# Optimization experiments

Hardware: AMD Instinct MI355X
Metric: run time of the kernel (lower is better)

## Reference

```python
import jax, jax.numpy as jnp
import numpy as np

NUM_CODES = 512
DIM = 64
B, M = 32, 64


def setup_inputs() -> dict:
    key = jax.random.key(0)
    k1, k2 = jax.random.split(key)
    inputs = jax.random.normal(k1, (B, M, M, DIM), dtype=jnp.float32)
    # keras 'uniform' initializer is U(-0.05, 0.05)
    embeddings = jax.random.uniform(k2, (NUM_CODES, DIM), dtype=jnp.float32,
                                    minval=-0.05, maxval=0.05)
    return {"inputs": inputs, "embeddings": embeddings}


def reference(inputs, embeddings):
    l2_inputs = jnp.sum(inputs * inputs, axis=-1, keepdims=True)      # [B,M,M,1]
    l2_embeddings = jnp.sum(embeddings * embeddings, axis=-1)          # [K]
    dot = jnp.einsum('bhwd,kd->bhwk', inputs, embeddings)              # [B,M,M,K]
    distance = l2_inputs + l2_embeddings - 2.0 * dot                   # [B,M,M,K]
    codes = jnp.argmin(distance, axis=-1).astype(jnp.int32)            # [B,M,M]
    code_vecs = embeddings[codes]                                      # [B,M,M,D]
    return codes, code_vecs
```

## Files before the change

kernel.cpp:

```cpp
#include <hip/hip_runtime.h>

#define NUM_CODES 512
#define DIM 64
#define NPIX (32 * 64 * 64)
#define CT (NUM_CODES / 16)
#define BLK 256
#define PPB 64

typedef __attribute__((ext_vector_type(8))) short bf16x8;
typedef __attribute__((ext_vector_type(4))) float f32x4;

__device__ __forceinline__ unsigned short f2bf(float f) {
    unsigned u = __float_as_uint(f);
    return (unsigned short)((u + 0x7fffu + ((u >> 16) & 1u)) >> 16);
}
__device__ __forceinline__ float bf2f(unsigned short h) {
    return __uint_as_float(((unsigned)h) << 16);
}

__global__ __launch_bounds__(256) void prep_kernel(
    const float* __restrict__ emb, unsigned short* __restrict__ AH,
    unsigned short* __restrict__ ALO, float* __restrict__ l2e,
    float* __restrict__ l2eh) {
    const int t = blockIdx.x * 256 + threadIdx.x;
    const int e0 = t * 4;
    const int c = e0 >> 6, d0 = e0 & 63;
    const float4 v = *(const float4*)(emb + c * DIM + d0);
    float f[4] = {v.x, v.y, v.z, v.w};
    unsigned short h[4], l[4];
#pragma unroll
    for (int i = 0; i < 4; ++i) {
        h[i] = f2bf(f[i]);
        l[i] = f2bf(f[i] - bf2f(h[i]));
    }
    const int ct = c >> 4, mr = c & 15, s = d0 >> 5, q = (d0 & 31) >> 3,
              j0 = d0 & 7;
    const int base = ((ct * 2 + s) * 64 + (q * 16 + mr)) * 8 + j0;
    *(ushort4*)(AH + base) = make_ushort4(h[0], h[1], h[2], h[3]);
    *(ushort4*)(ALO + base) = make_ushort4(l[0], l[1], l[2], l[3]);

    if (t < NUM_CODES) {
        const float* e = emb + t * DIM;
        float r[8];
#pragma unroll
        for (int j = 0; j < 8; ++j) {
            float w = e[j];
            r[j] = w * w;
        }
#pragma unroll
        for (int i = 8; i < DIM; i += 8)
#pragma unroll
            for (int j = 0; j < 8; ++j) {
                float w = e[i + j];
                r[j] += w * w;
            }
        float sv =
            ((r[0] + r[1]) + (r[2] + r[3])) + ((r[4] + r[5]) + (r[6] + r[7]));
        l2e[t] = sv;
        l2eh[t] = 0.5f * sv;
    }
}

__global__ __launch_bounds__(BLK) void vq_main(
    const float* __restrict__ x_in, const unsigned short* __restrict__ AH,
    const unsigned short* __restrict__ ALO, const float* __restrict__ l2e,
    const float* __restrict__ l2eh, const float* __restrict__ emb,
    float* __restrict__ codes_out, float* __restrict__ vecs_out) {
    __shared__ float s_l2eh[NUM_CODES];
    __shared__ float s_l2ex[NUM_CODES];
    __shared__ int s_top[PPB][2];
    __shared__ int s_code[PPB];

    const int tid = threadIdx.x, lane = tid & 63, wave = tid >> 6;
    s_l2eh[tid] = l2eh[tid];
    s_l2eh[tid + 256] = l2eh[tid + 256];
    s_l2ex[tid] = l2e[tid];
    s_l2ex[tid + 256] = l2e[tid + 256];
    __syncthreads();

    const int pg = blockIdx.x * PPB + wave * 16;
    const int p = lane & 15, q = lane >> 4;

    const float* xb = x_in + (size_t)(pg + p) * DIM + q * 8;
    float4 u0 = *(const float4*)(xb);
    float4 u1 = *(const float4*)(xb + 4);
    float4 u2 = *(const float4*)(xb + 32);
    float4 u3 = *(const float4*)(xb + 36);
    float f0[8] = {u0.x, u0.y, u0.z, u0.w, u1.x, u1.y, u1.z, u1.w};
    float f1[8] = {u2.x, u2.y, u2.z, u2.w, u3.x, u3.y, u3.z, u3.w};
    bf16x8 b0h, b0l, b1h, b1l;
#pragma unroll
    for (int j = 0; j < 8; ++j) {
        unsigned short hh = f2bf(f0[j]);
        b0h[j] = (short)hh;
        b0l[j] = (short)f2bf(f0[j] - bf2f(hh));
        unsigned short h2 = f2bf(f1[j]);
        b1h[j] = (short)h2;
        b1l[j] = (short)f2bf(f1[j] - bf2f(h2));
    }

    const int rowbase = q * 4;
    float d1 = 3.4e38f, d2 = 3.4e38f;
    int k1 = 0, k2 = 0;

    const unsigned short* pAH = AH + lane * 8;
    const unsigned short* pAL = ALO + lane * 8;
    for (int ct = 0; ct < CT; ++ct) {
        bf16x8 a0h = *(const bf16x8*)(pAH + ct * 1024);
        bf16x8 a0l = *(const bf16x8*)(pAL + ct * 1024);
        bf16x8 a1h = *(const bf16x8*)(pAH + ct * 1024 + 512);
        bf16x8 a1l = *(const bf16x8*)(pAL + ct * 1024 + 512);
        f32x4 acc = {0.f, 0.f, 0.f, 0.f};
        acc = __builtin_amdgcn_mfma_f32_16x16x32_bf16(a0h, b0h, acc, 0, 0, 0);
        acc = __builtin_amdgcn_mfma_f32_16x16x32_bf16(a1h, b1h, acc, 0, 0, 0);
        acc = __builtin_amdgcn_mfma_f32_16x16x32_bf16(a0l, b0h, acc, 0, 0, 0);
        acc = __builtin_amdgcn_mfma_f32_16x16x32_bf16(a1l, b1h, acc, 0, 0, 0);
        acc = __builtin_amdgcn_mfma_f32_16x16x32_bf16(a0h, b0l, acc, 0, 0, 0);
        acc = __builtin_amdgcn_mfma_f32_16x16x32_bf16(a1h, b1l, acc, 0, 0, 0);

        const int kb = ct * 16 + rowbase;
#pragma unroll
        for (int r = 0; r < 4; ++r) {
            const float d = s_l2eh[kb + r] - acc[r];
            const int kk = kb + r;
            const bool c = d < d1, c2 = d < d2;
            const float nd2 = c2 ? d : d2;
            const int nk2 = c2 ? kk : k2;
            d2 = c ? d1 : nd2;
            k2 = c ? k1 : nk2;
            k1 = c ? kk : k1;
            d1 = c ? d : d1;
        }
    }

#pragma unroll
    for (int off = 16; off <= 32; off <<= 1) {
        const float od1 = __shfl_xor(d1, off);
        const int ok1 = __shfl_xor(k1, off);
        const float od2 = __shfl_xor(d2, off);
        const int ok2 = __shfl_xor(k2, off);
        const bool c = od1 < d1;
        const float w1 = c ? od1 : d1;
        const int wk1 = c ? ok1 : k1;
        const float l1 = c ? d1 : od1;
        const int lk1 = c ? k1 : ok1;
        const bool cm = od2 < d2;
        const float m2 = cm ? od2 : d2;
        const int mk2 = cm ? ok2 : k2;
        const bool c3 = m2 < l1;
        d2 = c3 ? m2 : l1;
        k2 = c3 ? mk2 : lk1;
        d1 = w1;
        k1 = wk1;
    }
    if (lane < 16) {
        s_top[wave * 16 + lane][0] = k1;
        s_top[wave * 16 + lane][1] = k2;
    }
    __syncthreads();

    if (tid < PPB) {
        const int pix = blockIdx.x * PPB + tid;
        int ka = s_top[tid][0], kb2 = s_top[tid][1];
        if (kb2 < ka) {
            const int tt = ka;
            ka = kb2;
            kb2 = tt;
        }
        const float* xr = x_in + (size_t)pix * DIM;
        float x[DIM];
#pragma unroll
        for (int jj = 0; jj < 16; ++jj) {
            const float4 v = *(const float4*)(xr + jj * 4);
            x[4 * jj + 0] = v.x;
            x[4 * jj + 1] = v.y;
            x[4 * jj + 2] = v.z;
            x[4 * jj + 3] = v.w;
        }
        float r[8];
#pragma unroll
        for (int j = 0; j < 8; ++j) r[j] = x[j] * x[j];
#pragma unroll
        for (int i = 8; i < DIM; i += 8)
#pragma unroll
            for (int j = 0; j < 8; ++j) r[j] += x[i + j] * x[i + j];
        const float l2x =
            ((r[0] + r[1]) + (r[2] + r[3])) + ((r[4] + r[5]) + (r[6] + r[7]));

        const float* ea = emb + (size_t)ka * DIM;
        float acca = 0.f;
#pragma unroll
        for (int d = 0; d < DIM; ++d) acca = __builtin_fmaf(x[d], ea[d], acca);
        const float da = (l2x + s_l2ex[ka]) - 2.0f * acca;

        const float* eb = emb + (size_t)kb2 * DIM;
        float accb = 0.f;
#pragma unroll
        for (int d = 0; d < DIM; ++d) accb = __builtin_fmaf(x[d], eb[d], accb);
        const float db = (l2x + s_l2ex[kb2]) - 2.0f * accb;

        const int sel = (db < da) ? kb2 : ka;
        s_code[tid] = sel;
        codes_out[pix] = (float)sel;
    }
    __syncthreads();

    const float4* emb4 = (const float4*)emb;
    float4* vout4 = (float4*)(vecs_out + (size_t)blockIdx.x * PPB * DIM);
#pragma unroll
    for (int it = 0; it < (PPB * DIM / 4) / BLK; ++it) {
        const int fidx = tid + it * BLK;
        const int pp = fidx >> 4, dd = fidx & 15;
        vout4[fidx] = emb4[(size_t)s_code[pp] * (DIM / 4) + dd];
    }
}

extern "C" void kernel_launch(void* const* d_in, const int* in_sizes, int n_in,
                              void* d_out, int out_size, void* d_ws,
                              size_t ws_size, hipStream_t stream) {
    const float* x_in = (const float*)d_in[0];
    const float* emb = (const float*)d_in[1];

    unsigned short* AH = (unsigned short*)d_ws;
    unsigned short* ALO = AH + NUM_CODES * DIM;
    float* l2e = (float*)(ALO + NUM_CODES * DIM);
    float* l2eh = l2e + NUM_CODES;

    float* codes_out = (float*)d_out;
    float* vecs_out = (float*)d_out + NPIX;

    hipLaunchKernelGGL(prep_kernel, dim3(32), dim3(256), 0, stream, emb, AH,
                       ALO, l2e, l2eh);
    hipLaunchKernelGGL(vq_main, dim3(NPIX / PPB), dim3(BLK), 0, stream, x_in,
                       AH, ALO, l2e, l2eh, emb, codes_out, vecs_out);
}
```

Baseline: 131.7 us.

## Process four pixel groups per wave to reuse codebook fragments across MFMAs

Each wave now handles four 16-pixel groups instead of one, so every codebook A-fragment load and LDS norm read is shared by four groups of MFMAs. The block covers 256 pixels, and all 256 threads take part in the exact fp32 rescoring of the top-2 candidates instead of only 64. This cuts global/L2 traffic for the codebook and idle threads in the refine stage. In exchange, register pressure rises from holding four sets of B fragments and top-2 state, the grid shrinks fourfold, and launch_bounds asks for 2 blocks per SIMD group.

New measurement: 127.9 us. -2.9%, faster.

```diff
diff --git a/kernel.cpp b/kernel.cpp
--- a/kernel.cpp
+++ b/kernel.cpp
@@ -5,7 +5,8 @@
 #define NPIX (32 * 64 * 64)
 #define CT (NUM_CODES / 16)
 #define BLK 256
-#define PPB 64
+#define NGRP 4
+#define PPB 256
 
 typedef __attribute__((ext_vector_type(8))) short bf16x8;
 typedef __attribute__((ext_vector_type(4))) float f32x4;
@@ -61,7 +62,7 @@
     }
 }
 
-__global__ __launch_bounds__(BLK) void vq_main(
+__global__ __launch_bounds__(BLK, 2) void vq_main(
     const float* __restrict__ x_in, const unsigned short* __restrict__ AH,
     const unsigned short* __restrict__ ALO, const float* __restrict__ l2e,
     const float* __restrict__ l2eh, const float* __restrict__ emb,
@@ -78,88 +79,110 @@
     s_l2ex[tid + 256] = l2e[tid + 256];
     __syncthreads();
 
-    const int pg = blockIdx.x * PPB + wave * 16;
     const int p = lane & 15, q = lane >> 4;
-
-    const float* xb = x_in + (size_t)(pg + p) * DIM + q * 8;
-    float4 u0 = *(const float4*)(xb);
-    float4 u1 = *(const float4*)(xb + 4);
-    float4 u2 = *(const float4*)(xb + 32);
-    float4 u3 = *(const float4*)(xb + 36);
-    float f0[8] = {u0.x, u0.y, u0.z, u0.w, u1.x, u1.y, u1.z, u1.w};
-    float f1[8] = {u2.x, u2.y, u2.z, u2.w, u3.x, u3.y, u3.z, u3.w};
-    bf16x8 b0h, b0l, b1h, b1l;
-#pragma unroll
-    for (int j = 0; j < 8; ++j) {
-        unsigned short hh = f2bf(f0[j]);
-        b0h[j] = (short)hh;
-        b0l[j] = (short)f2bf(f0[j] - bf2f(hh));
-        unsigned short h2 = f2bf(f1[j]);
-        b1h[j] = (short)h2;
-        b1l[j] = (short)f2bf(f1[j] - bf2f(h2));
+    const int pw = blockIdx.x * PPB + wave * (16 * NGRP);
+
+    bf16x8 bh0[NGRP], bl0[NGRP], bh1[NGRP], bl1[NGRP];
+#pragma unroll
+    for (int g = 0; g < NGRP; ++g) {
+        const float* xb = x_in + (size_t)(pw + g * 16 + p) * DIM + q * 8;
+        float4 u0 = *(const float4*)(xb);
+        float4 u1 = *(const float4*)(xb + 4);
+        float4 u2 = *(const float4*)(xb + 32);
+        float4 u3 = *(const float4*)(xb + 36);
+        float f0[8] = {u0.x, u0.y, u0.z, u0.w, u1.x, u1.y, u1.z, u1.w};
+        float f1[8] = {u2.x, u2.y, u2.z, u2.w, u3.x, u3.y, u3.z, u3.w};
+#pragma unroll
+        for (int j = 0; j < 8; ++j) {
+            unsigned short hh = f2bf(f0[j]);
+            bh0[g][j] = (short)hh;
+            bl0[g][j] = (short)f2bf(f0[j] - bf2f(hh));
+            unsigned short h2 = f2bf(f1[j]);
+            bh1[g][j] = (short)h2;
+            bl1[g][j] = (short)f2bf(f1[j] - bf2f(h2));
+        }
     }
 
     const int rowbase = q * 4;
-    float d1 = 3.4e38f, d2 = 3.4e38f;
-    int k1 = 0, k2 = 0;
+    float d1[NGRP], d2[NGRP];
+    int k1[NGRP], k2[NGRP];
+#pragma unroll
+    for (int g = 0; g < NGRP; ++g) {
+        d1[g] = 3.4e38f;
+        d2[g] = 3.4e38f;
+        k1[g] = 0;
+        k2[g] = 0;
+    }
 
     const unsigned short* pAH = AH + lane * 8;
     const unsigned short* pAL = ALO + lane * 8;
     for (int ct = 0; ct < CT; ++ct) {
-        bf16x8 a0h = *(const bf16x8*)(pAH + ct * 1024);
-        bf16x8 a0l = *(const bf16x8*)(pAL + ct * 1024);
-        bf16x8 a1h = *(const bf16x8*)(pAH + ct * 1024 + 512);
-        bf16x8 a1l = *(const bf16x8*)(pAL + ct * 1024 + 512);
-        f32x4 acc = {0.f, 0.f, 0.f, 0.f};
-        acc = __builtin_amdgcn_mfma_f32_16x16x32_bf16(a0h, b0h, acc, 0, 0, 0);
-        acc = __builtin_amdgcn_mfma_f32_16x16x32_bf16(a1h, b1h, acc, 0, 0, 0);
-        acc = __builtin_amdgcn_mfma_f32_16x16x32_bf16(a0l, b0h, acc, 0, 0, 0);
-        acc = __builtin_amdgcn_mfma_f32_16x16x32_bf16(a1l, b1h, acc, 0, 0, 0);
-        acc = __builtin_amdgcn_mfma_f32_16x16x32_bf16(a0h, b0l, acc, 0, 0, 0);
-        acc = __builtin_amdgcn_mfma_f32_16x16x32_bf16(a1h, b1l, acc, 0, 0, 0);
-
+        const bf16x8 a0h = *(const bf16x8*)(pAH + ct * 1024);
+        const bf16x8 a0l = *(const bf16x8*)(pAL + ct * 1024);
+        const bf16x8 a1h = *(const bf16x8*)(pAH + ct * 1024 + 512);
+        const bf16x8 a1l = *(const bf16x8*)(pAL + ct * 1024 + 512);
         const int kb = ct * 16 + rowbase;
-#pragma unroll
-        for (int r = 0; r < 4; ++r) {
-            const float d = s_l2eh[kb + r] - acc[r];
-            const int kk = kb + r;
-            const bool c = d < d1, c2 = d < d2;
-            const float nd2 = c2 ? d : d2;
-            const int nk2 = c2 ? kk : k2;
-            d2 = c ? d1 : nd2;
-            k2 = c ? k1 : nk2;
-            k1 = c ? kk : k1;
-            d1 = c ? d : d1;
-        }
-    }
-
-#pragma unroll
-    for (int off = 16; off <= 32; off <<= 1) {
-        const float od1 = __shfl_xor(d1, off);
-        const int ok1 = __shfl_xor(k1, off);
-        const float od2 = __shfl_xor(d2, off);
-        const int ok2 = __shfl_xor(k2, off);
-        const bool c = od1 < d1;
-        const float w1 = c ? od1 : d1;
-        const int wk1 = c ? ok1 : k1;
-        const float l1 = c ? d1 : od1;
-        const int lk1 = c ? k1 : ok1;
-        const bool cm = od2 < d2;
-        const float m2 = cm ? od2 : d2;
-        const int mk2 = cm ? ok2 : k2;
-        const bool c3 = m2 < l1;
-        d2 = c3 ? m2 : l1;
-        k2 = c3 ? mk2 : lk1;
-        d1 = w1;
-        k1 = wk1;
-    }
-    if (lane < 16) {
-        s_top[wave * 16 + lane][0] = k1;
-        s_top[wave * 16 + lane][1] = k2;
+        float l2v[4];
+#pragma unroll
+        for (int r = 0; r < 4; ++r) l2v[r] = s_l2eh[kb + r];
+
+#pragma unroll
+        for (int g = 0; g < NGRP; ++g) {
+            f32x4 acc = {0.f, 0.f, 0.f, 0.f};
+            acc = __builtin_amdgcn_mfma_f32_16x16x32_bf16(a0h, bh0[g], acc, 0, 0, 0);
+            acc = __builtin_amdgcn_mfma_f32_16x16x32_bf16(a1h, bh1[g], acc, 0, 0, 0);
+            acc = __builtin_amdgcn_mfma_f32_16x16x32_bf16(a0l, bh0[g], acc, 0, 0, 0);
+            acc = __builtin_amdgcn_mfma_f32_16x16x32_bf16(a1l, bh1[g], acc, 0, 0, 0);
+            acc = __builtin_amdgcn_mfma_f32_16x16x32_bf16(a0h, bl0[g], acc, 0, 0, 0);
+            acc = __builtin_amdgcn_mfma_f32_16x16x32_bf16(a1h, bl1[g], acc, 0, 0, 0);
+
+#pragma unroll
+            for (int r = 0; r < 4; ++r) {
+                const float d = l2v[r] - acc[r];
+                const int kk = kb + r;
+                const bool c = d < d1[g], c2 = d < d2[g];
+                const float nd2 = c2 ? d : d2[g];
+                const int nk2 = c2 ? kk : k2[g];
+                d2[g] = c ? d1[g] : nd2;
+                k2[g] = c ? k1[g] : nk2;
+                k1[g] = c ? kk : k1[g];
+                d1[g] = c ? d : d1[g];
+            }
+        }
+    }
+
+#pragma unroll
+    for (int g = 0; g < NGRP; ++g) {
+        float a1 = d1[g], a2 = d2[g];
+        int b1 = k1[g], b2 = k2[g];
+#pragma unroll
+        for (int off = 16; off <= 32; off <<= 1) {
+            const float od1 = __shfl_xor(a1, off);
+            const int ok1 = __shfl_xor(b1, off);
+            const float od2 = __shfl_xor(a2, off);
+            const int ok2 = __shfl_xor(b2, off);
+            const bool c = od1 < a1;
+            const float w1 = c ? od1 : a1;
+            const int wk1 = c ? ok1 : b1;
+            const float l1 = c ? a1 : od1;
+            const int lk1 = c ? b1 : ok1;
+            const bool cm = od2 < a2;
+            const float m2 = cm ? od2 : a2;
+            const int mk2 = cm ? ok2 : b2;
+            const bool c3 = m2 < l1;
+            a2 = c3 ? m2 : l1;
+            b2 = c3 ? mk2 : lk1;
+            a1 = w1;
+            b1 = wk1;
+        }
+        if (lane < 16) {
+            s_top[wave * (16 * NGRP) + g * 16 + lane][0] = b1;
+            s_top[wave * (16 * NGRP) + g * 16 + lane][1] = b2;
+        }
     }
     __syncthreads();
 
-    if (tid < PPB) {
+    {
         const int pix = blockIdx.x * PPB + tid;
         int ka = s_top[tid][0], kb2 = s_top[tid][1];
         if (kb2 < ka) {
```
